# Kernel tuning notes

Measured on AMD Instinct MI355X. Metric: run time of the kernel, lower is better.

## Reference

```python
import jax, jax.numpy as jnp
import numpy as np

B, N, OBS_DIM = 64, 512, 128
HIDDEN_DIM, MESSAGE_DIM, ACTION_DIM = 256, 128, 16


def _dense_params(key, din, dout):
    kw, kb = jax.random.split(key)
    W = jax.random.normal(kw, (din, dout), jnp.float32) * 0.02
    b = jnp.zeros((dout,), jnp.float32)
    return W, b


def setup_inputs() -> dict:
    key = jax.random.key(0)
    ks = jax.random.split(key, 12)
    obs_batch = jax.random.normal(ks[0], (B, N, OBS_DIM), jnp.float32)
    dones_batch = jnp.zeros((B, N), jnp.bool_)
    We, be = _dense_params(ks[1], OBS_DIM, HIDDEN_DIM)
    Wc, bc = _dense_params(ks[2], HIDDEN_DIM, MESSAGE_DIM // 4)
    Wn, bn = _dense_params(ks[3], HIDDEN_DIM, MESSAGE_DIM // 2)
    Wb, bb = _dense_params(ks[4], HIDDEN_DIM, MESSAGE_DIM // 4)
    Wi, bi = _dense_params(ks[5], HIDDEN_DIM, 1)
    Wq, bq = _dense_params(ks[6], HIDDEN_DIM, MESSAGE_DIM)
    Wk, bk = _dense_params(ks[7], MESSAGE_DIM, MESSAGE_DIM)
    Wv, bv = _dense_params(ks[8], MESSAGE_DIM, MESSAGE_DIM)
    Wp, bp = _dense_params(ks[9], HIDDEN_DIM + MESSAGE_DIM, HIDDEN_DIM)
    Wa, ba = _dense_params(ks[10], HIDDEN_DIM, ACTION_DIM)
    Wcr, bcr = _dense_params(ks[11], HIDDEN_DIM, 1)
    return {"obs_batch": obs_batch, "dones_batch": dones_batch,
            "We": We, "be": be, "Wc": Wc, "bc": bc, "Wn": Wn, "bn": bn,
            "Wb": Wb, "bb": bb, "Wi": Wi, "bi": bi, "Wq": Wq, "bq": bq,
            "Wk": Wk, "bk": bk, "Wv": Wv, "bv": bv, "Wp": Wp, "bp": bp,
            "Wa": Wa, "ba": ba, "Wcr": Wcr, "bcr": bcr}


def reference(obs_batch, dones_batch, We, be, Wc, bc, Wn, bn, Wb, bb, Wi, bi,
              Wq, bq, Wk, bk, Wv, bv, Wp, bp, Wa, ba, Wcr, bcr):
    dense = lambda x, W, b: x @ W + b
    encoded = jax.nn.relu(dense(obs_batch, We, be))                 # [B,N,H]
    messages = jnp.concatenate([dense(encoded, Wc, bc),
                                dense(encoded, Wn, bn),
                                dense(encoded, Wb, bb)], axis=-1)   # [B,N,M]
    importance = jax.nn.sigmoid(dense(encoded, Wi, bi))             # [B,N,1]
    Q = dense(encoded, Wq, bq)
    K = dense(messages, Wk, bk)
    V = dense(messages, Wv, bv)
    scores = jnp.einsum('bqd,bkd->bqk', Q, K) / jnp.sqrt(jnp.float32(MESSAGE_DIM))
    importance_weights = importance * jnp.transpose(importance, (0, 2, 1))  # [B,N,N]
    scores = scores * importance_weights
    norms = jnp.linalg.norm(obs_batch, axis=-1, keepdims=True)      # [B,N,1]
    obs_sim = jnp.einsum('bid,bjd->bij', obs_batch, obs_batch)
    obs_sim = obs_sim / (norms + 1e-08)
    obs_sim = obs_sim / (jnp.transpose(norms, (0, 2, 1)) + 1e-08)
    scores = scores + obs_sim * 0.5
    attn = jax.nn.softmax(scores, axis=-1)
    aggregated = jnp.einsum('bqk,bkd->bqd', attn, V)                # [B,N,M]
    combined = jnp.concatenate([encoded, aggregated], axis=-1)
    x = jax.nn.relu(dense(combined, Wp, bp))
    logits = dense(x, Wa, ba)
    value = dense(x, Wcr, bcr).squeeze(-1)
    return (logits, value)
```

## Files before the change

### kernel.cpp

```cpp
#include <hip/hip_runtime.h>
#include <math.h>


typedef __attribute__((ext_vector_type(8))) short short8;
typedef __attribute__((ext_vector_type(4))) float f32x4;

#define RSQRT_D 0.08838834764831843f

__device__ __forceinline__ unsigned short f2bf(float f) {
  union { float f; unsigned u; } v; v.f = f;
  return (unsigned short)((v.u + 0x7FFFu + ((v.u >> 16) & 1u)) >> 16);
}
__device__ __forceinline__ float bf2f(unsigned short h) {
  union { unsigned u; float f; } v; v.u = ((unsigned)h) << 16;
  return v.f;
}
__device__ __forceinline__ unsigned pack2(float a, float b) {
  return (unsigned)f2bf(a) | ((unsigned)f2bf(b) << 16);
}

__device__ __forceinline__ int swz(int row, int chunk) {
  return row * 128 + ((chunk ^ ((row & 7) << 1)) << 3);
}

__global__ __launch_bounds__(256) void prep_w(
    const float* __restrict__ We, const float* __restrict__ Wq,
    const float* __restrict__ Wk, const float* __restrict__ Wv,
    const float* __restrict__ Wp, const float* __restrict__ Wc,
    const float* __restrict__ Wn, const float* __restrict__ Wb,
    const float* __restrict__ bc, const float* __restrict__ bn,
    const float* __restrict__ bb, const float* __restrict__ Wa,
    const float* __restrict__ Wcr, unsigned short* __restrict__ WeT,
    unsigned short* __restrict__ Wmq, unsigned short* __restrict__ Wkv,
    unsigned short* __restrict__ WpT, unsigned short* __restrict__ WaCrT,
    float* __restrict__ bm) {
  int idx = blockIdx.x * 256 + threadIdx.x;
  if (idx < 32768) {
    int n = idx >> 7, k = idx & 127;
    WeT[idx] = f2bf(We[k * 256 + n]);
  } else if (idx < 65536) {
    int i = idx - 32768;
    int d = i >> 8, h = i & 255;
    float v = (d < 32)   ? Wc[h * 32 + d]
            : (d < 96)   ? Wn[h * 64 + (d - 32)]
                         : Wb[h * 32 + (d - 96)];
    Wmq[i] = f2bf(v);
  } else if (idx < 98304) {
    int i = idx - 65536;
    int n = i >> 8, k = i & 255;
    Wmq[32768 + i] = f2bf(Wq[k * 128 + n]);
  } else if (idx < 114688) {
    int i = idx - 98304;
    int n = i >> 7, k = i & 127;
    Wkv[i] = f2bf(Wk[k * 128 + n]);
  } else if (idx < 131072) {
    int i = idx - 114688;
    int n = i >> 7, k = i & 127;
    Wkv[16384 + i] = f2bf(Wv[k * 128 + n]);
  } else if (idx < 229376) {
    int i = idx - 131072;
    int n = i / 384, k = i - n * 384;
    WpT[i] = f2bf(Wp[k * 256 + n]);
  } else if (idx < 237568) {
    int i = idx - 229376;
    int n = i >> 8, k = i & 255;
    float v = (n < 16) ? Wa[k * 16 + n] : (n == 16) ? Wcr[k] : 0.f;
    WaCrT[i] = f2bf(v);
  } else if (idx < 237696) {
    int i = idx - 237568;
    bm[i] = (i < 32) ? bc[i] : (i < 96) ? bn[i - 32] : bb[i - 96];
  }
}

__global__ __launch_bounds__(256) void prep_obs(
    const float* __restrict__ obs, unsigned short* __restrict__ obs_bf,
    unsigned short* __restrict__ As, unsigned short* __restrict__ Bs) {
  int t = blockIdx.x * 4 + (threadIdx.x >> 6);
  int lane = threadIdx.x & 63;
  const float* row = obs + (size_t)t * 128;
  float2 o = *(const float2*)(row + lane * 2);
  float s2 = o.x * o.x + o.y * o.y;
#pragma unroll
  for (int off = 1; off < 64; off <<= 1) s2 += __shfl_xor(s2, off);
  float inv = 1.f / (sqrtf(s2) + 1e-8f);
  ((unsigned*)obs_bf)[(size_t)t * 64 + lane] = pack2(o.x, o.y);
  ((unsigned*)As)[(size_t)t * 128 + 64 + lane] =
      pack2(o.x * 0.5f * inv, o.y * 0.5f * inv);
  ((unsigned*)Bs)[(size_t)t * 128 + 64 + lane] = pack2(o.x * inv, o.y * inv);
}

__global__ __launch_bounds__(256) void imp_kernel(
    const unsigned short* __restrict__ enc, const float* __restrict__ Wi,
    const float* __restrict__ bi, float* __restrict__ impA,
    float* __restrict__ impB) {
  int t = blockIdx.x * 4 + (threadIdx.x >> 6);
  int lane = threadIdx.x & 63;
  const unsigned* eu = (const unsigned*)(enc + (size_t)t * 256);
  unsigned u0 = eu[lane * 2], u1 = eu[lane * 2 + 1];
  float4 w = *(const float4*)(Wi + lane * 4);
  float s = bf2f((unsigned short)(u0 & 0xFFFF)) * w.x +
            bf2f((unsigned short)(u0 >> 16)) * w.y +
            bf2f((unsigned short)(u1 & 0xFFFF)) * w.z +
            bf2f((unsigned short)(u1 >> 16)) * w.w;
#pragma unroll
  for (int off = 1; off < 64; off <<= 1) s += __shfl_xor(s, off);
  if (lane == 0) {
    float sg = 1.0f / (1.0f + __expf(-(s + bi[0])));
    impA[t] = sg * RSQRT_D;
    impB[t] = sg;
  }
}

template <int MODE>
__device__ __forceinline__ void epi_store(unsigned short* out, int ldc,
                                          const float* bias,
                                          const float* scale, int rowb,
                                          int col, const f32x4& a) {
  const float bv = bias ? bias[col] : 0.f;
  if constexpr (MODE == 3) {
    unsigned short t0 = f2bf(a[0] + bv), t1 = f2bf(a[1] + bv);
    unsigned short t2 = f2bf(a[2] + bv), t3 = f2bf(a[3] + bv);
    uint2 o;
    o.x = (unsigned)t0 | ((unsigned)t1 << 16);
    o.y = (unsigned)t2 | ((unsigned)t3 << 16);
    *(uint2*)(out + ((size_t)(rowb >> 9) * 128 + col) * 512 + (rowb & 511)) = o;
  } else {
#pragma unroll
    for (int r = 0; r < 4; ++r) {
      float v = a[r] + bv;
      if constexpr (MODE == 1) v = fmaxf(v, 0.f);
      if constexpr (MODE == 2) v *= scale[rowb + r];
      out[(size_t)(rowb + r) * ldc + col] = f2bf(v);
    }
  }
}

template <int M0, int M1>
__global__ __launch_bounds__(256, 2) void gemm_dual(
    const unsigned short* __restrict__ A1, int lda1, int K1,
    const unsigned short* __restrict__ A2, int lda2, int Ktot,
    const unsigned short* __restrict__ Bt, int ldb,
    const float* __restrict__ bias0, const float* __restrict__ bias1,
    const float* __restrict__ scale, unsigned short* __restrict__ out0,
    int ldc0, unsigned short* __restrict__ out1, int ldc1, int xsplit) {
  __shared__ unsigned short Asr[64][72];
  __shared__ unsigned short Bsr[128][72];
  const int tid = threadIdx.x;
  const int lane = tid & 63, wave = tid >> 6;
  const int quad = lane >> 4, l16 = lane & 15;
  const int wm = wave & 1, wn = wave >> 1;
  const int bm = blockIdx.y * 64, bn = blockIdx.x * 128;

  f32x4 acc[2][4];
#pragma unroll
  for (int i = 0; i < 2; ++i)
#pragma unroll
    for (int j = 0; j < 4; ++j) acc[i][j] = (f32x4){0.f, 0.f, 0.f, 0.f};

  const int ar = tid >> 3, ac = tid & 7;
  for (int kt = 0; kt < Ktot; kt += 64) {
    const unsigned short* Asrc;
    int lda, kloc;
    if (kt < K1) { Asrc = A1; lda = lda1; kloc = kt; }
    else         { Asrc = A2; lda = lda2; kloc = kt - K1; }
#pragma unroll
    for (int it = 0; it < 2; ++it) {
      int r = ar + it * 32;
      uint4 v = *(const uint4*)(Asrc + (size_t)(bm + r) * lda + kloc + ac * 8);
      *(uint4*)&Asr[r][ac * 8] = v;
    }
#pragma unroll
    for (int it = 0; it < 4; ++it) {
      int r = ar + it * 32;
      uint4 v = *(const uint4*)(Bt + (size_t)(bn + r) * ldb + kt + ac * 8);
      *(uint4*)&Bsr[r][ac * 8] = v;
    }
    __syncthreads();
#pragma unroll
    for (int ks = 0; ks < 64; ks += 32) {
      short8 af[2], bfr[4];
#pragma unroll
      for (int i = 0; i < 2; ++i)
        af[i] = *(const short8*)&Asr[wm * 32 + i * 16 + l16][ks + quad * 8];
#pragma unroll
      for (int j = 0; j < 4; ++j)
        bfr[j] = *(const short8*)&Bsr[wn * 64 + j * 16 + l16][ks + quad * 8];
#pragma unroll
      for (int i = 0; i < 2; ++i)
#pragma unroll
        for (int j = 0; j < 4; ++j)
          acc[i][j] = __builtin_amdgcn_mfma_f32_16x16x32_bf16(af[i], bfr[j],
                                                              acc[i][j], 0, 0, 0);
    }
    __syncthreads();
  }
  const int colb = bn + wn * 64 + l16;
#pragma unroll
  for (int i = 0; i < 2; ++i) {
    const int rowb = bm + wm * 32 + i * 16 + quad * 4;
#pragma unroll
    for (int j = 0; j < 4; ++j) {
      const int col = colb + j * 16;
      if (col < xsplit)
        epi_store<M0>(out0, ldc0, bias0, scale, rowb, col, acc[i][j]);
      else
        epi_store<M1>(out1, ldc1, bias1, scale, rowb, col - xsplit, acc[i][j]);
    }
  }
}

__global__ __launch_bounds__(256, 3) void flash2(
    const unsigned short* __restrict__ As, const unsigned short* __restrict__ Bs,
    const unsigned short* __restrict__ vT, unsigned short* __restrict__ agg) {
  __shared__ unsigned short Ub[128 * 128];
  __shared__ unsigned short Pp[32 * 128];
  __shared__ float redm[2][32];
  __shared__ float reds[2][32];
  const int tid = threadIdx.x;
  const int lane = tid & 63, wave = tid >> 6;
  const int quad = lane >> 4, l16 = lane & 15;
  const int wm = wave & 1, wn = wave >> 1;
  const int b = blockIdx.x & 63;
  const int qt = blockIdx.x >> 6;
  const size_t tokA = (size_t)b * 512 + qt * 32;

  short8 af[8];
#pragma unroll
  for (int kc = 0; kc < 8; ++kc)
    af[kc] = *(const short8*)(As + (tokA + wm * 16 + l16) * 256 + kc * 32 +
                              quad * 8);

  f32x4 s[4][4];
#pragma unroll
  for (int kt = 0; kt < 4; ++kt)
#pragma unroll
    for (int nt = 0; nt < 4; ++nt) s[kt][nt] = (f32x4){0.f, 0.f, 0.f, 0.f};

  const int lr = tid >> 4, lc = tid & 15;

#pragma unroll
  for (int kt = 0; kt < 4; ++kt) {
#pragma unroll
    for (int kh = 0; kh < 2; ++kh) {
      __syncthreads();
#pragma unroll
      for (int it = 0; it < 8; ++it) {
        int r = lr + it * 16;
        *(uint4*)&Ub[swz(r, lc)] =
            *(const uint4*)(Bs + ((size_t)b * 512 + kt * 128 + r) * 256 +
                            kh * 128 + lc * 8);
      }
      __syncthreads();
#pragma unroll
      for (int kk = 0; kk < 4; ++kk) {
        short8 bfr[4];
#pragma unroll
        for (int nt = 0; nt < 4; ++nt) {
          int rrow = wn * 64 + nt * 16 + l16;
          bfr[nt] = *(const short8*)&Ub[swz(rrow, kk * 4 + quad)];
        }
#pragma unroll
        for (int nt = 0; nt < 4; ++nt)
          s[kt][nt] = __builtin_amdgcn_mfma_f32_16x16x32_bf16(
              af[kh * 4 + kk], bfr[nt], s[kt][nt], 0, 0, 0);
      }
    }
  }

  const int rbase = wm * 16 + quad * 4;
  float mt4[4];
#pragma unroll
  for (int r = 0; r < 4; ++r) {
    float mv = -1e30f;
#pragma unroll
    for (int kt = 0; kt < 4; ++kt)
#pragma unroll
      for (int nt = 0; nt < 4; ++nt) mv = fmaxf(mv, s[kt][nt][r]);
#pragma unroll
    for (int off = 1; off < 16; off <<= 1) mv = fmaxf(mv, __shfl_xor(mv, off));
    mt4[r] = mv;
  }
  if (l16 == 0) {
#pragma unroll
    for (int r = 0; r < 4; ++r) redm[wn][rbase + r] = mt4[r];
  }
  __syncthreads();
  float lsum[4];
#pragma unroll
  for (int r = 0; r < 4; ++r) {
    float mfull = fmaxf(mt4[r], redm[1 ^ wn][rbase + r]);
    float sum = 0.f;
#pragma unroll
    for (int kt = 0; kt < 4; ++kt)
#pragma unroll
      for (int nt = 0; nt < 4; ++nt) {
        float p = __expf(s[kt][nt][r] - mfull);
        s[kt][nt][r] = p;
        sum += p;
      }
#pragma unroll
    for (int off = 1; off < 16; off <<= 1) sum += __shfl_xor(sum, off);
    lsum[r] = sum;
  }
  if (l16 == 0) {
#pragma unroll
    for (int r = 0; r < 4; ++r) reds[wn][rbase + r] = lsum[r];
  }
  __syncthreads();
  float linv[4];
#pragma unroll
  for (int r = 0; r < 4; ++r)
    linv[r] = 1.0f / (lsum[r] + reds[1 ^ wn][rbase + r]);

  f32x4 oacc[4];
#pragma unroll
  for (int nt = 0; nt < 4; ++nt) oacc[nt] = (f32x4){0.f, 0.f, 0.f, 0.f};
#pragma unroll
  for (int vt = 0; vt < 4; ++vt) {
    __syncthreads();
#pragma unroll
    for (int nt = 0; nt < 4; ++nt)
#pragma unroll
      for (int r = 0; r < 4; ++r) {
        int row = rbase + r;
        int col = wn * 64 + nt * 16 + l16;
        Pp[row * 128 + (((col >> 3) ^ ((row & 7) << 1)) << 3) + (col & 7)] =
            f2bf(s[vt][nt][r]);
      }
#pragma unroll
    for (int it = 0; it < 8; ++it) {
      int r = lr + it * 16;
      *(uint4*)&Ub[swz(r, lc)] =
          *(const uint4*)(vT + ((size_t)b * 128 + r) * 512 + vt * 128 + lc * 8);
    }
    __syncthreads();
#pragma unroll
    for (int kk = 0; kk < 4; ++kk) {
      short8 pa = *(const short8*)&Pp[swz(wm * 16 + l16, kk * 4 + quad)];
#pragma unroll
      for (int nt = 0; nt < 4; ++nt) {
        int rrow = wn * 64 + nt * 16 + l16;
        short8 vb = *(const short8*)&Ub[swz(rrow, kk * 4 + quad)];
        oacc[nt] = __builtin_amdgcn_mfma_f32_16x16x32_bf16(pa, vb, oacc[nt],
                                                           0, 0, 0);
      }
    }
  }

#pragma unroll
  for (int nt = 0; nt < 4; ++nt) {
    const int col = wn * 64 + nt * 16 + l16;
#pragma unroll
    for (int r = 0; r < 4; ++r)
      agg[(tokA + rbase + r) * 128 + col] = f2bf(oacc[nt][r] * linv[r]);
  }
}

__global__ __launch_bounds__(256, 3) void xh_gemm(
    const unsigned short* __restrict__ A1, const unsigned short* __restrict__ A2,
    const unsigned short* __restrict__ WpT, const float* __restrict__ bp,
    const unsigned short* __restrict__ WaCrT, const float* __restrict__ ba,
    const float* __restrict__ bcr, float* __restrict__ logits,
    float* __restrict__ value) {
  __shared__ unsigned short Asr[32][72];
  __shared__ unsigned short Bsr[256][72];
  const int tid = threadIdx.x;
  const int lane = tid & 63, wave = tid >> 6;
  const int quad = lane >> 4, l16 = lane & 15;
  const int bm = blockIdx.x * 32;

  f32x4 acc[2][4];
#pragma unroll
  for (int i = 0; i < 2; ++i)
#pragma unroll
    for (int j = 0; j < 4; ++j) acc[i][j] = (f32x4){0.f, 0.f, 0.f, 0.f};

  const int ar = tid >> 3, ac = tid & 7;
  for (int kt = 0; kt < 384; kt += 64) {
    const unsigned short* Asrc;
    int lda, kloc;
    if (kt < 256) { Asrc = A1; lda = 256; kloc = kt; }
    else          { Asrc = A2; lda = 128; kloc = kt - 256; }
    *(uint4*)&Asr[ar][ac * 8] =
        *(const uint4*)(Asrc + (size_t)(bm + ar) * lda + kloc + ac * 8);
#pragma unroll
    for (int it = 0; it < 8; ++it) {
      int idx = tid + it * 256;
      int r = idx >> 3, c = idx & 7;
      *(uint4*)&Bsr[r][c * 8] = *(const uint4*)(WpT + (size_t)r * 384 + kt + c * 8);
    }
    __syncthreads();
#pragma unroll
    for (int kk = 0; kk < 2; ++kk) {
      short8 afr[2], bfr[4];
#pragma unroll
      for (int i = 0; i < 2; ++i)
        afr[i] = *(const short8*)&Asr[i * 16 + l16][kk * 32 + quad * 8];
#pragma unroll
      for (int j = 0; j < 4; ++j)
        bfr[j] = *(const short8*)&Bsr[wave * 64 + j * 16 + l16][kk * 32 + quad * 8];
#pragma unroll
      for (int i = 0; i < 2; ++i)
#pragma unroll
        for (int j = 0; j < 4; ++j)
          acc[i][j] = __builtin_amdgcn_mfma_f32_16x16x32_bf16(afr[i], bfr[j],
                                                              acc[i][j], 0, 0, 0);
    }
    __syncthreads();
  }
  unsigned short* xs = &Bsr[0][0];
#pragma unroll
  for (int i = 0; i < 2; ++i) {
    const int row = i * 16 + quad * 4;
#pragma unroll
    for (int j = 0; j < 4; ++j) {
      const int col = wave * 64 + j * 16 + l16;
      const float bv = bp[col];
#pragma unroll
      for (int r = 0; r < 4; ++r)
        xs[(row + r) * 264 + col] = f2bf(fmaxf(acc[i][j][r] + bv, 0.f));
    }
  }
  __syncthreads();
  const int wm2 = wave & 1, wn2 = wave >> 1;
  f32x4 hacc = (f32x4){0.f, 0.f, 0.f, 0.f};
#pragma unroll
  for (int kk = 0; kk < 8; ++kk) {
    short8 pa = *(const short8*)&xs[(wm2 * 16 + l16) * 264 + kk * 32 + quad * 8];
    short8 wb = *(const short8*)(WaCrT + (size_t)(wn2 * 16 + l16) * 256 +
                                 kk * 32 + quad * 8);
    hacc = __builtin_amdgcn_mfma_f32_16x16x32_bf16(pa, wb, hacc, 0, 0, 0);
  }
  const int n = wn2 * 16 + l16;
#pragma unroll
  for (int r = 0; r < 4; ++r) {
    const size_t tok = bm + wm2 * 16 + quad * 4 + r;
    if (n < 16)
      logits[tok * 16 + n] = hacc[r] + ba[n];
    else if (n == 16)
      value[tok] = hacc[r] + bcr[0];
  }
}

extern "C" void kernel_launch(void* const* d_in, const int* in_sizes, int n_in,
                              void* d_out, int out_size, void* d_ws,
                              size_t ws_size, hipStream_t stream) {
  const float* obs = (const float*)d_in[0];
  const float* We = (const float*)d_in[2];
  const float* be = (const float*)d_in[3];
  const float* Wc = (const float*)d_in[4];
  const float* bc = (const float*)d_in[5];
  const float* Wn = (const float*)d_in[6];
  const float* bn = (const float*)d_in[7];
  const float* Wb = (const float*)d_in[8];
  const float* bb = (const float*)d_in[9];
  const float* Wi = (const float*)d_in[10];
  const float* bi = (const float*)d_in[11];
  const float* Wq = (const float*)d_in[12];
  const float* bq = (const float*)d_in[13];
  const float* Wk = (const float*)d_in[14];
  const float* bk = (const float*)d_in[15];
  const float* Wv = (const float*)d_in[16];
  const float* bv = (const float*)d_in[17];
  const float* Wp = (const float*)d_in[18];
  const float* bp = (const float*)d_in[19];
  const float* Wa = (const float*)d_in[20];
  const float* ba = (const float*)d_in[21];
  const float* Wcr = (const float*)d_in[22];
  const float* bcr = (const float*)d_in[23];

  char* base = (char*)d_ws;
  unsigned short* enc_bf = (unsigned short*)(base);
  unsigned short* As     = (unsigned short*)(base + 16777216);
  unsigned short* Bs     = (unsigned short*)(base + 33554432);
  unsigned short* obsagg = (unsigned short*)(base + 50331648);
  unsigned short* msg_bf = (unsigned short*)(base + 58720256);
  unsigned short* vT     = (unsigned short*)(base + 75497472);
  float* impA            = (float*)(base + 83886080);
  float* impB            = (float*)(base + 84017152);
  unsigned short* WeT    = (unsigned short*)(base + 84148224);
  unsigned short* Wmq    = (unsigned short*)(base + 84213760);
  unsigned short* Wkv    = (unsigned short*)(base + 84344832);
  unsigned short* WpT    = (unsigned short*)(base + 84410368);
  float* bmb             = (float*)(base + 84606976);
  unsigned short* WaCrT  = (unsigned short*)(base + 84607488);

  prep_w<<<929, 256, 0, stream>>>(We, Wq, Wk, Wv, Wp, Wc, Wn, Wb, bc, bn, bb,
                                  Wa, Wcr, WeT, Wmq, Wkv, WpT, WaCrT, bmb);
  prep_obs<<<8192, 256, 0, stream>>>(obs, obsagg, As, Bs);

  gemm_dual<1, 1><<<dim3(2, 512), 256, 0, stream>>>(
      obsagg, 128, 128, nullptr, 0, 128, WeT, 128, be, be, nullptr, enc_bf,
      256, enc_bf, 256, 256);
  imp_kernel<<<8192, 256, 0, stream>>>(enc_bf, Wi, bi, impA, impB);

  gemm_dual<0, 2><<<dim3(2, 512), 256, 0, stream>>>(
      enc_bf, 256, 256, nullptr, 0, 256, Wmq, 256, bmb, bq, impA, msg_bf, 128,
      As, 256, 128);
  gemm_dual<2, 3><<<dim3(2, 512), 256, 0, stream>>>(
      msg_bf, 128, 128, nullptr, 0, 128, Wkv, 128, bk, bv, impB, Bs, 256, vT,
      0, 128);

  flash2<<<1024, 256, 0, stream>>>(As, Bs, vT, obsagg);

  xh_gemm<<<1024, 256, 0, stream>>>(enc_bf, obsagg, WpT, bp, WaCrT, ba, bcr,
                                    (float*)d_out, (float*)d_out + 524288);
}
```

Baseline: 223.2 us.

## Fuse prep kernels, fold importance into encoder GEMM, use direct-to-LDS loads

Merges the weight prep, obs prep, and output/importance initialisation into one launch. The encoder GEMM epilogue now computes the importance dot product and accumulates it with atomics, which removes the separate importance kernel; downstream GEMMs apply the sigmoid themselves. All GEMMs move to 128x128 tiles with global_load_lds into XOR-swizzled LDS, and the final projection splits N across blocks, atomically accumulating partial head outputs onto bias-initialised logits and value. The atomics make summation order nondeterministic, and the larger tiles halve the grid size.

```diff
diff --git a/kernel.cpp b/kernel.cpp
--- a/kernel.cpp
+++ b/kernel.cpp
@@ -6,237 +6,246 @@
 typedef __attribute__((ext_vector_type(4))) float f32x4;
 
 #define RSQRT_D 0.08838834764831843f
+#define MFMA __builtin_amdgcn_mfma_f32_16x16x32_bf16
 
 __device__ __forceinline__ unsigned short f2bf(float f) {
   union { float f; unsigned u; } v; v.f = f;
   return (unsigned short)((v.u + 0x7FFFu + ((v.u >> 16) & 1u)) >> 16);
 }
-__device__ __forceinline__ float bf2f(unsigned short h) {
-  union { unsigned u; float f; } v; v.u = ((unsigned)h) << 16;
-  return v.f;
-}
 __device__ __forceinline__ unsigned pack2(float a, float b) {
   return (unsigned)f2bf(a) | ((unsigned)f2bf(b) << 16);
 }
-
-__device__ __forceinline__ int swz(int row, int chunk) {
-  return row * 128 + ((chunk ^ ((row & 7) << 1)) << 3);
-}
-
-__global__ __launch_bounds__(256) void prep_w(
-    const float* __restrict__ We, const float* __restrict__ Wq,
-    const float* __restrict__ Wk, const float* __restrict__ Wv,
-    const float* __restrict__ Wp, const float* __restrict__ Wc,
-    const float* __restrict__ Wn, const float* __restrict__ Wb,
-    const float* __restrict__ bc, const float* __restrict__ bn,
-    const float* __restrict__ bb, const float* __restrict__ Wa,
-    const float* __restrict__ Wcr, unsigned short* __restrict__ WeT,
-    unsigned short* __restrict__ Wmq, unsigned short* __restrict__ Wkv,
-    unsigned short* __restrict__ WpT, unsigned short* __restrict__ WaCrT,
-    float* __restrict__ bm) {
-  int idx = blockIdx.x * 256 + threadIdx.x;
-  if (idx < 32768) {
-    int n = idx >> 7, k = idx & 127;
-    WeT[idx] = f2bf(We[k * 256 + n]);
-  } else if (idx < 65536) {
-    int i = idx - 32768;
-    int d = i >> 8, h = i & 255;
-    float v = (d < 32)   ? Wc[h * 32 + d]
-            : (d < 96)   ? Wn[h * 64 + (d - 32)]
-                         : Wb[h * 32 + (d - 96)];
-    Wmq[i] = f2bf(v);
-  } else if (idx < 98304) {
-    int i = idx - 65536;
-    int n = i >> 8, k = i & 255;
-    Wmq[32768 + i] = f2bf(Wq[k * 128 + n]);
-  } else if (idx < 114688) {
-    int i = idx - 98304;
-    int n = i >> 7, k = i & 127;
-    Wkv[i] = f2bf(Wk[k * 128 + n]);
-  } else if (idx < 131072) {
-    int i = idx - 114688;
-    int n = i >> 7, k = i & 127;
-    Wkv[16384 + i] = f2bf(Wv[k * 128 + n]);
-  } else if (idx < 229376) {
-    int i = idx - 131072;
-    int n = i / 384, k = i - n * 384;
-    WpT[i] = f2bf(Wp[k * 256 + n]);
-  } else if (idx < 237568) {
-    int i = idx - 229376;
-    int n = i >> 8, k = i & 255;
-    float v = (n < 16) ? Wa[k * 16 + n] : (n == 16) ? Wcr[k] : 0.f;
-    WaCrT[i] = f2bf(v);
-  } else if (idx < 237696) {
-    int i = idx - 237568;
-    bm[i] = (i < 32) ? bc[i] : (i < 96) ? bn[i - 32] : bb[i - 96];
-  }
-}
-
-__global__ __launch_bounds__(256) void prep_obs(
-    const float* __restrict__ obs, unsigned short* __restrict__ obs_bf,
-    unsigned short* __restrict__ As, unsigned short* __restrict__ Bs) {
-  int t = blockIdx.x * 4 + (threadIdx.x >> 6);
-  int lane = threadIdx.x & 63;
-  const float* row = obs + (size_t)t * 128;
-  float2 o = *(const float2*)(row + lane * 2);
-  float s2 = o.x * o.x + o.y * o.y;
-#pragma unroll
-  for (int off = 1; off < 64; off <<= 1) s2 += __shfl_xor(s2, off);
-  float inv = 1.f / (sqrtf(s2) + 1e-8f);
-  ((unsigned*)obs_bf)[(size_t)t * 64 + lane] = pack2(o.x, o.y);
-  ((unsigned*)As)[(size_t)t * 128 + 64 + lane] =
-      pack2(o.x * 0.5f * inv, o.y * 0.5f * inv);
-  ((unsigned*)Bs)[(size_t)t * 128 + 64 + lane] = pack2(o.x * inv, o.y * inv);
-}
-
-__global__ __launch_bounds__(256) void imp_kernel(
-    const unsigned short* __restrict__ enc, const float* __restrict__ Wi,
-    const float* __restrict__ bi, float* __restrict__ impA,
-    float* __restrict__ impB) {
-  int t = blockIdx.x * 4 + (threadIdx.x >> 6);
-  int lane = threadIdx.x & 63;
-  const unsigned* eu = (const unsigned*)(enc + (size_t)t * 256);
-  unsigned u0 = eu[lane * 2], u1 = eu[lane * 2 + 1];
-  float4 w = *(const float4*)(Wi + lane * 4);
-  float s = bf2f((unsigned short)(u0 & 0xFFFF)) * w.x +
-            bf2f((unsigned short)(u0 >> 16)) * w.y +
-            bf2f((unsigned short)(u1 & 0xFFFF)) * w.z +
-            bf2f((unsigned short)(u1 >> 16)) * w.w;
-#pragma unroll
-  for (int off = 1; off < 64; off <<= 1) s += __shfl_xor(s, off);
-  if (lane == 0) {
-    float sg = 1.0f / (1.0f + __expf(-(s + bi[0])));
-    impA[t] = sg * RSQRT_D;
-    impB[t] = sg;
-  }
-}
-
-template <int MODE>
-__device__ __forceinline__ void epi_store(unsigned short* out, int ldc,
-                                          const float* bias,
-                                          const float* scale, int rowb,
-                                          int col, const f32x4& a) {
-  const float bv = bias ? bias[col] : 0.f;
+__device__ __forceinline__ short8 ld8(const unsigned short* p) {
+  return *(const short8*)p;
+}
+__device__ __forceinline__ void gl16(const unsigned short* g,
+                                     unsigned short* l) {
+  __builtin_amdgcn_global_load_lds(
+      (const __attribute__((address_space(1))) unsigned int*)(const void*)g,
+      (__attribute__((address_space(3))) unsigned int*)(void*)l, 16, 0, 0);
+}
+
+__global__ __launch_bounds__(256) void prep_all(
+    const float* __restrict__ obs, const float* __restrict__ We,
+    const float* __restrict__ Wq, const float* __restrict__ Wk,
+    const float* __restrict__ Wv, const float* __restrict__ Wp,
+    const float* __restrict__ Wc, const float* __restrict__ Wn,
+    const float* __restrict__ Wb, const float* __restrict__ bc,
+    const float* __restrict__ bn, const float* __restrict__ bb,
+    const float* __restrict__ Wa, const float* __restrict__ Wcr,
+    const float* __restrict__ ba, const float* __restrict__ bcr,
+    unsigned short* __restrict__ WeT, unsigned short* __restrict__ Wmq,
+    unsigned short* __restrict__ Wkv, unsigned short* __restrict__ WpT,
+    unsigned short* __restrict__ WaCrT, float* __restrict__ bm,
+    unsigned short* __restrict__ obs_bf, unsigned short* __restrict__ As,
+    unsigned short* __restrict__ Bs, float* __restrict__ logits,
+    float* __restrict__ value, float* __restrict__ imp_raw) {
+  const int bid = blockIdx.x, tid = threadIdx.x;
+  if (bid < 929) {
+    int idx = bid * 256 + tid;
+    if (idx < 32768) {
+      int n = idx >> 7, k = idx & 127;
+      WeT[idx] = f2bf(We[k * 256 + n]);
+    } else if (idx < 65536) {
+      int i = idx - 32768;
+      int d = i >> 8, h = i & 255;
+      float v = (d < 32)   ? Wc[h * 32 + d]
+              : (d < 96)   ? Wn[h * 64 + (d - 32)]
+                           : Wb[h * 32 + (d - 96)];
+      Wmq[i] = f2bf(v);
+    } else if (idx < 98304) {
+      int i = idx - 65536;
+      int n = i >> 8, k = i & 255;
+      Wmq[32768 + i] = f2bf(Wq[k * 128 + n]);
+    } else if (idx < 114688) {
+      int i = idx - 98304;
+      int n = i >> 7, k = i & 127;
+      Wkv[i] = f2bf(Wk[k * 128 + n]);
+    } else if (idx < 131072) {
+      int i = idx - 114688;
+      int n = i >> 7, k = i & 127;
+      Wkv[16384 + i] = f2bf(Wv[k * 128 + n]);
+    } else if (idx < 229376) {
+      int i = idx - 131072;
+      int n = i / 384, k = i - n * 384;
+      WpT[i] = f2bf(Wp[k * 256 + n]);
+    } else if (idx < 237568) {
+      int i = idx - 229376;
+      int n = i >> 8, k = i & 255;
+      float v = (n < 16) ? Wa[k * 16 + n] : (n == 16) ? Wcr[k] : 0.f;
+      WaCrT[i] = f2bf(v);
+    } else if (idx < 237696) {
+      int i = idx - 237568;
+      bm[i] = (i < 32) ? bc[i] : (i < 96) ? bn[i - 32] : bb[i - 96];
+    }
+  } else if (bid < 9121) {
+    int t = (bid - 929) * 4 + (tid >> 6);
+    int lane = tid & 63;
+    const float* row = obs + (size_t)t * 128;
+    float2 o = *(const float2*)(row + lane * 2);
+    float s2 = o.x * o.x + o.y * o.y;
+#pragma unroll
+    for (int off = 1; off < 64; off <<= 1) s2 += __shfl_xor(s2, off);
+    float inv = 1.f / (sqrtf(s2) + 1e-8f);
+    ((unsigned*)obs_bf)[(size_t)t * 64 + lane] = pack2(o.x, o.y);
+    ((unsigned*)As)[(size_t)t * 128 + 64 + lane] =
+        pack2(o.x * 0.5f * inv, o.y * 0.5f * inv);
+    ((unsigned*)Bs)[(size_t)t * 128 + 64 + lane] = pack2(o.x * inv, o.y * inv);
+  } else if (bid < 11297) {
+    int i = (bid - 9121) * 256 + tid;
+    if (i < 524288) logits[i] = ba[i & 15];
+    else value[i - 524288] = bcr[0];
+  } else {
+    imp_raw[(bid - 11297) * 256 + tid] = 0.f;
+  }
+}
+
+template <int MODE, int IMP>
+__device__ __forceinline__ void emit(unsigned short* out, int ldc,
+                                     const float* bias, const float* sg,
+                                     int rowb, int col, const f32x4& a,
+                                     float* ip, const float* Wi, int gcol) {
+  const float bv = bias[col];
   if constexpr (MODE == 3) {
-    unsigned short t0 = f2bf(a[0] + bv), t1 = f2bf(a[1] + bv);
-    unsigned short t2 = f2bf(a[2] + bv), t3 = f2bf(a[3] + bv);
     uint2 o;
-    o.x = (unsigned)t0 | ((unsigned)t1 << 16);
-    o.y = (unsigned)t2 | ((unsigned)t3 << 16);
+    o.x = pack2(a[0] + bv, a[1] + bv);
+    o.y = pack2(a[2] + bv, a[3] + bv);
     *(uint2*)(out + ((size_t)(rowb >> 9) * 128 + col) * 512 + (rowb & 511)) = o;
   } else {
+    float wv = 0.f;
+    if constexpr (IMP) wv = Wi[gcol];
 #pragma unroll
     for (int r = 0; r < 4; ++r) {
       float v = a[r] + bv;
       if constexpr (MODE == 1) v = fmaxf(v, 0.f);
-      if constexpr (MODE == 2) v *= scale[rowb + r];
+      if constexpr (MODE == 2) v *= sg[r];
       out[(size_t)(rowb + r) * ldc + col] = f2bf(v);
-    }
-  }
-}
-
-template <int M0, int M1>
-__global__ __launch_bounds__(256, 2) void gemm_dual(
+      if constexpr (IMP) ip[r] += v * wv;
+    }
+  }
+}
+
+template <int M0, int M1, int IMP>
+__global__ __launch_bounds__(256, 2) void gemm_t(
     const unsigned short* __restrict__ A1, int lda1, int K1,
     const unsigned short* __restrict__ A2, int lda2, int Ktot,
     const unsigned short* __restrict__ Bt, int ldb,
     const float* __restrict__ bias0, const float* __restrict__ bias1,
-    const float* __restrict__ scale, unsigned short* __restrict__ out0,
-    int ldc0, unsigned short* __restrict__ out1, int ldc1, int xsplit) {
-  __shared__ unsigned short Asr[64][72];
-  __shared__ unsigned short Bsr[128][72];
-  const int tid = threadIdx.x;
-  const int lane = tid & 63, wave = tid >> 6;
+    const float* __restrict__ raw, const float* __restrict__ bi, float mult,
+    const float* __restrict__ Wi, float* __restrict__ imp_out,
+    unsigned short* __restrict__ out0, int ldc0,
+    unsigned short* __restrict__ out1, int ldc1, int xsplit) {
+  __shared__ unsigned short Asr[8192];
+  __shared__ unsigned short Bsr[8192];
+  const int tid = threadIdx.x, lane = tid & 63, wave = tid >> 6;
   const int quad = lane >> 4, l16 = lane & 15;
   const int wm = wave & 1, wn = wave >> 1;
-  const int bm = blockIdx.y * 64, bn = blockIdx.x * 128;
-
-  f32x4 acc[2][4];
-#pragma unroll
-  for (int i = 0; i < 2; ++i)
+  const int bm = blockIdx.y * 128, bn = blockIdx.x * 128;
+  const int srow = tid >> 3, slc = tid & 7;
+
+  f32x4 acc[4][4];
+#pragma unroll
+  for (int i = 0; i < 4; ++i)
 #pragma unroll
     for (int j = 0; j < 4; ++j) acc[i][j] = (f32x4){0.f, 0.f, 0.f, 0.f};
 
-  const int ar = tid >> 3, ac = tid & 7;
   for (int kt = 0; kt < Ktot; kt += 64) {
-    const unsigned short* Asrc;
+    const unsigned short* Ap;
     int lda, kloc;
-    if (kt < K1) { Asrc = A1; lda = lda1; kloc = kt; }
-    else         { Asrc = A2; lda = lda2; kloc = kt - K1; }
-#pragma unroll
-    for (int it = 0; it < 2; ++it) {
-      int r = ar + it * 32;
-      uint4 v = *(const uint4*)(Asrc + (size_t)(bm + r) * lda + kloc + ac * 8);
-      *(uint4*)&Asr[r][ac * 8] = v;
-    }
-#pragma unroll
-    for (int it = 0; it < 4; ++it) {
-      int r = ar + it * 32;
-      uint4 v = *(const uint4*)(Bt + (size_t)(bn + r) * ldb + kt + ac * 8);
-      *(uint4*)&Bsr[r][ac * 8] = v;
+    if (kt < K1) { Ap = A1; lda = lda1; kloc = kt; }
+    else         { Ap = A2; lda = lda2; kloc = kt - K1; }
+#pragma unroll
+    for (int i = 0; i < 4; ++i) {
+      int row = i * 32 + srow;
+      gl16(Ap + (size_t)(bm + row) * lda + kloc + ((slc ^ (row & 7)) << 3),
+           Asr + i * 2048 + wave * 512);
+      gl16(Bt + (size_t)(bn + row) * ldb + kt + ((slc ^ (row & 7)) << 3),
+           Bsr + i * 2048 + wave * 512);
     }
     __syncthreads();
 #pragma unroll
-    for (int ks = 0; ks < 64; ks += 32) {
-      short8 af[2], bfr[4];
-#pragma unroll
-      for (int i = 0; i < 2; ++i)
-        af[i] = *(const short8*)&Asr[wm * 32 + i * 16 + l16][ks + quad * 8];
-#pragma unroll
-      for (int j = 0; j < 4; ++j)
-        bfr[j] = *(const short8*)&Bsr[wn * 64 + j * 16 + l16][ks + quad * 8];
-#pragma unroll
-      for (int i = 0; i < 2; ++i)
-#pragma unroll
-        for (int j = 0; j < 4; ++j)
-          acc[i][j] = __builtin_amdgcn_mfma_f32_16x16x32_bf16(af[i], bfr[j],
-                                                              acc[i][j], 0, 0, 0);
+    for (int ks = 0; ks < 2; ++ks) {
+      short8 af[4], bf[4];
+#pragma unroll
+      for (int mi = 0; mi < 4; ++mi) {
+        int row = wm * 64 + mi * 16 + l16;
+        af[mi] = *(const short8*)&Asr[row * 64 + (((ks * 4 + quad) ^ (row & 7)) << 3)];
+      }
+#pragma unroll
+      for (int ni = 0; ni < 4; ++ni) {
+        int row = wn * 64 + ni * 16 + l16;
+        bf[ni] = *(const short8*)&Bsr[row * 64 + (((ks * 4 + quad) ^ (row & 7)) << 3)];
+      }
+#pragma unroll
+      for (int mi = 0; mi < 4; ++mi)
+#pragma unroll
+        for (int ni = 0; ni < 4; ++ni)
+          acc[mi][ni] = MFMA(af[mi], bf[ni], acc[mi][ni], 0, 0, 0);
     }
     __syncthreads();
   }
-  const int colb = bn + wn * 64 + l16;
-#pragma unroll
-  for (int i = 0; i < 2; ++i) {
-    const int rowb = bm + wm * 32 + i * 16 + quad * 4;
-#pragma unroll
-    for (int j = 0; j < 4; ++j) {
-      const int col = colb + j * 16;
+
+  float bi0 = 0.f;
+  if constexpr (M0 == 2 || M1 == 2) bi0 = bi[0];
+#pragma unroll
+  for (int mi = 0; mi < 4; ++mi) {
+    const int rowb = bm + wm * 64 + mi * 16 + quad * 4;
+    float sg[4] = {0.f, 0.f, 0.f, 0.f};
+    if constexpr (M0 == 2 || M1 == 2) {
+#pragma unroll
+      for (int r = 0; r < 4; ++r)
+        sg[r] = mult / (1.f + __expf(-(raw[rowb + r] + bi0)));
+    }
+    float ip[4] = {0.f, 0.f, 0.f, 0.f};
+#pragma unroll
+    for (int ni = 0; ni < 4; ++ni) {
+      const int col = bn + wn * 64 + ni * 16 + l16;
       if (col < xsplit)
-        epi_store<M0>(out0, ldc0, bias0, scale, rowb, col, acc[i][j]);
+        emit<M0, IMP>(out0, ldc0, bias0, sg, rowb, col, acc[mi][ni], ip, Wi, col);
       else
-        epi_store<M1>(out1, ldc1, bias1, scale, rowb, col - xsplit, acc[i][j]);
-    }
-  }
-}
-
-__global__ __launch_bounds__(256, 3) void flash2(
+        emit<M1, 0>(out1, ldc1, bias1, sg, rowb, col - xsplit, acc[mi][ni],
+                    nullptr, nullptr, 0);
+    }
+    if constexpr (IMP) {
+#pragma unroll
+      for (int r = 0; r < 4; ++r) {
+#pragma unroll
+        for (int off = 1; off < 16; off <<= 1)
+          ip[r] += __shfl_xor(ip[r], off);
+      }
+      if (l16 == 0) {
+#pragma unroll
+        for (int r = 0; r < 4; ++r) atomicAdd(&imp_out[rowb + r], ip[r]);
+      }
+    }
+  }
+}
+
+__global__ __launch_bounds__(256, 3) void flash4(
     const unsigned short* __restrict__ As, const unsigned short* __restrict__ Bs,
     const unsigned short* __restrict__ vT, unsigned short* __restrict__ agg) {
-  __shared__ unsigned short Ub[128 * 128];
-  __shared__ unsigned short Pp[32 * 128];
+  __shared__ unsigned short Ub[16384];
+  __shared__ unsigned short Pp[4096];
   __shared__ float redm[2][32];
   __shared__ float reds[2][32];
-  const int tid = threadIdx.x;
-  const int lane = tid & 63, wave = tid >> 6;
+  const int tid = threadIdx.x, lane = tid & 63, wave = tid >> 6;
   const int quad = lane >> 4, l16 = lane & 15;
   const int wm = wave & 1, wn = wave >> 1;
   const int b = blockIdx.x & 63;
   const int qt = blockIdx.x >> 6;
-  const size_t tokA = (size_t)b * 512 + qt * 32;
+  const size_t tok0 = (size_t)b * 512 + qt * 32;
+  const int srow = tid >> 4, slc = tid & 15;
 
   short8 af[8];
 #pragma unroll
   for (int kc = 0; kc < 8; ++kc)
-    af[kc] = *(const short8*)(As + (tokA + wm * 16 + l16) * 256 + kc * 32 +
-                              quad * 8);
+    af[kc] = ld8(As + (tok0 + wm * 16 + l16) * 256 + kc * 32 + quad * 8);
 
   f32x4 s[4][4];
 #pragma unroll
   for (int kt = 0; kt < 4; ++kt)
 #pragma unroll
     for (int nt = 0; nt < 4; ++nt) s[kt][nt] = (f32x4){0.f, 0.f, 0.f, 0.f};
-
-  const int lr = tid >> 4, lc = tid & 15;
 
 #pragma unroll
   for (int kt = 0; kt < 4; ++kt) {
@@ -244,11 +253,11 @@
     for (int kh = 0; kh < 2; ++kh) {
       __syncthreads();
 #pragma unroll
-      for (int it = 0; it < 8; ++it) {
-        int r = lr + it * 16;
-        *(uint4*)&Ub[swz(r, lc)] =
-            *(const uint4*)(Bs + ((size_t)b * 512 + kt * 128 + r) * 256 +
-                            kh * 128 + lc * 8);
+      for (int i = 0; i < 8; ++i) {
+        int row = i * 16 + srow;
+        gl16(Bs + ((size_t)b * 512 + kt * 128 + row) * 256 + kh * 128 +
+                 ((slc ^ (row & 15)) << 3),
+             Ub + i * 2048 + wave * 512);
       }
       __syncthreads();
 #pragma unroll
@@ -256,19 +265,18 @@
         short8 bfr[4];
 #pragma unroll
         for (int nt = 0; nt < 4; ++nt) {
-          int rrow = wn * 64 + nt * 16 + l16;
-          bfr[nt] = *(const short8*)&Ub[swz(rrow, kk * 4 + quad)];
+          int rr = wn * 64 + nt * 16 + l16;
+          bfr[nt] = *(const short8*)&Ub[rr * 128 + (((kk * 4 + quad) ^ (rr & 15)) << 3)];
         }
 #pragma unroll
         for (int nt = 0; nt < 4; ++nt)
-          s[kt][nt] = __builtin_amdgcn_mfma_f32_16x16x32_bf16(
-              af[kh * 4 + kk], bfr[nt], s[kt][nt], 0, 0, 0);
+          s[kt][nt] = MFMA(af[kh * 4 + kk], bfr[nt], s[kt][nt], 0, 0, 0);
       }
     }
   }
 
   const int rbase = wm * 16 + quad * 4;
-  float mt4[4];
+  float mt[4];
 #pragma unroll
   for (int r = 0; r < 4; ++r) {
     float mv = -1e30f;
@@ -278,17 +286,17 @@
       for (int nt = 0; nt < 4; ++nt) mv = fmaxf(mv, s[kt][nt][r]);
 #pragma unroll
     for (int off = 1; off < 16; off <<= 1) mv = fmaxf(mv, __shfl_xor(mv, off));
-    mt4[r] = mv;
+    mt[r] = mv;
   }
   if (l16 == 0) {
 #pragma unroll
-    for (int r = 0; r < 4; ++r) redm[wn][rbase + r] = mt4[r];
+    for (int r = 0; r < 4; ++r) redm[wn][rbase + r] = mt[r];
   }
   __syncthreads();
   float lsum[4];
 #pragma unroll
   for (int r = 0; r < 4; ++r) {
-    float mfull = fmaxf(mt4[r], redm[1 ^ wn][rbase + r]);
+    float mfull = fmaxf(mt[r], redm[1 ^ wn][rbase + r]);
     float sum = 0.f;
 #pragma unroll
     for (int kt = 0; kt < 4; ++kt)
@@ -319,126 +327,153 @@
   for (int vt = 0; vt < 4; ++vt) {
     __syncthreads();
 #pragma unroll
-    for (int nt = 0; nt < 4; ++nt)
+    for (int nt = 0; nt < 4; ++nt) {
+      const int col = wn * 64 + nt * 16 + l16;
 #pragma unroll
       for (int r = 0; r < 4; ++r) {
-        int row = rbase + r;
-        int col = wn * 64 + nt * 16 + l16;
-        Pp[row * 128 + (((col >> 3) ^ ((row & 7) << 1)) << 3) + (col & 7)] =
+        const int row = rbase + r;
+        Pp[row * 128 + (((col >> 3) ^ (row & 15)) << 3) + (col & 7)] =
             f2bf(s[vt][nt][r]);
       }
-#pragma unroll
-    for (int it = 0; it < 8; ++it) {
-      int r = lr + it * 16;
-      *(uint4*)&Ub[swz(r, lc)] =
-          *(const uint4*)(vT + ((size_t)b * 128 + r) * 512 + vt * 128 + lc * 8);
+    }
+#pragma unroll
+    for (int i = 0; i < 8; ++i) {
+      int row = i * 16 + srow;
+      gl16(vT + ((size_t)b * 128 + row) * 512 + vt * 128 +
+               ((slc ^ (row & 15)) << 3),
+           Ub + i * 2048 + wave * 512);
     }
     __syncthreads();
 #pragma unroll
     for (int kk = 0; kk < 4; ++kk) {
-      short8 pa = *(const short8*)&Pp[swz(wm * 16 + l16, kk * 4 + quad)];
+      const int prow = wm * 16 + l16;
+      short8 pa = *(const short8*)&Pp[prow * 128 + (((kk * 4 + quad) ^ (prow & 15)) << 3)];
 #pragma unroll
       for (int nt = 0; nt < 4; ++nt) {
-        int rrow = wn * 64 + nt * 16 + l16;
-        short8 vb = *(const short8*)&Ub[swz(rrow, kk * 4 + quad)];
-        oacc[nt] = __builtin_amdgcn_mfma_f32_16x16x32_bf16(pa, vb, oacc[nt],
-                                                           0, 0, 0);
-      }
-    }
-  }
-
+        int rr = wn * 64 + nt * 16 + l16;
+        short8 vb = *(const short8*)&Ub[rr * 128 + (((kk * 4 + quad) ^ (rr & 15)) << 3)];
+        oacc[nt] = MFMA(pa, vb, oacc[nt], 0, 0, 0);
+      }
+    }
+  }
 #pragma unroll
   for (int nt = 0; nt < 4; ++nt) {
     const int col = wn * 64 + nt * 16 + l16;
 #pragma unroll
     for (int r = 0; r < 4; ++r)
-      agg[(tokA + rbase + r) * 128 + col] = f2bf(oacc[nt][r] * linv[r]);
-  }
-}
-
-__global__ __launch_bounds__(256, 3) void xh_gemm(
-    const unsigned short* __restrict__ A1, const unsigned short* __restrict__ A2,
+      agg[(tok0 + rbase + r) * 128 + col] = f2bf(oacc[nt][r] * linv[r]);
+  }
+}
+
+__global__ __launch_bounds__(256, 2) void xh_gemm(
+    const unsigned short* __restrict__ enc, const unsigned short* __restrict__ agg,
     const unsigned short* __restrict__ WpT, const float* __restrict__ bp,
-    const unsigned short* __restrict__ WaCrT, const float* __restrict__ ba,
-    const float* __restrict__ bcr, float* __restrict__ logits,
+    const unsigned short* __restrict__ WaCrT, float* __restrict__ logits,
     float* __restrict__ value) {
-  __shared__ unsigned short Asr[32][72];
-  __shared__ unsigned short Bsr[256][72];
-  const int tid = threadIdx.x;
-  const int lane = tid & 63, wave = tid >> 6;
+  __shared__ unsigned short sm[16384];
+  unsigned short* Asr = sm;
+  unsigned short* Bsr = sm + 8192;
+  const int tid = threadIdx.x, lane = tid & 63, wave = tid >> 6;
   const int quad = lane >> 4, l16 = lane & 15;
-  const int bm = blockIdx.x * 32;
-
-  f32x4 acc[2][4];
+  const int wm = wave & 1, wn = wave >> 1;
+  const int bm = blockIdx.y * 128, bn = blockIdx.x * 128;
+  const int srow = tid >> 3, slc = tid & 7;
+
+  f32x4 acc[4][4];
+#pragma unroll
+  for (int i = 0; i < 4; ++i)
+#pragma unroll
+    for (int j = 0; j < 4; ++j) acc[i][j] = (f32x4){0.f, 0.f, 0.f, 0.f};
+
+  for (int kt = 0; kt < 384; kt += 64) {
+    const unsigned short* Ap;
+    int lda, kloc;
+    if (kt < 256) { Ap = enc; lda = 256; kloc = kt; }
+    else          { Ap = agg; lda = 128; kloc = kt - 256; }
+#pragma unroll
+    for (int i = 0; i < 4; ++i) {
+      int row = i * 32 + srow;
+      gl16(Ap + (size_t)(bm + row) * lda + kloc + ((slc ^ (row & 7)) << 3),
+           Asr + i * 2048 + wave * 512);
+      gl16(WpT + (size_t)(bn + row) * 384 + kt + ((slc ^ (row & 7)) << 3),
+           Bsr + i * 2048 + wave * 512);
+    }
+    __syncthreads();
+#pragma unroll
+    for (int ks = 0; ks < 2; ++ks) {
+      short8 af[4], bf[4];
+#pragma unroll
+      for (int mi = 0; mi < 4; ++mi) {
+        int row = wm * 64 + mi * 16 + l16;
+        af[mi] = *(const short8*)&Asr[row * 64 + (((ks * 4 + quad) ^ (row & 7)) << 3)];
+      }
+#pragma unroll
+      for (int ni = 0; ni < 4; ++ni) {
+        int row = wn * 64 + ni * 16 + l16;
+        bf[ni] = *(const short8*)&Bsr[row * 64 + (((ks * 4 + quad) ^ (row & 7)) << 3)];
+      }
+#pragma unroll
+      for (int mi = 0; mi < 4; ++mi)
+#pragma unroll
+        for (int ni = 0; ni < 4; ++ni)
+          acc[mi][ni] = MFMA(af[mi], bf[ni], acc[mi][ni], 0, 0, 0);
+    }
+    __syncthreads();
+  }
+
+#pragma unroll
+  for (int mi = 0; mi < 4; ++mi) {
+    const int row = wm * 64 + mi * 16 + quad * 4;
+#pragma unroll
+    for (int ni = 0; ni < 4; ++ni) {
+      const int colc = wn * 64 + ni * 16 + l16;
+      const float bv = bp[bn + colc];
+#pragma unroll
+      for (int r = 0; r < 4; ++r) {
+        float v = fmaxf(acc[mi][ni][r] + bv, 0.f);
+        sm[(row + r) * 128 + (((colc >> 3) ^ ((row + r) & 15)) << 3) + (colc & 7)] =
+            f2bf(v);
+      }
+    }
+  }
+  __syncthreads();
+
+  f32x4 h[2][2];
 #pragma unroll
   for (int i = 0; i < 2; ++i)
 #pragma unroll
-    for (int j = 0; j < 4; ++j) acc[i][j] = (f32x4){0.f, 0.f, 0.f, 0.f};
-
-  const int ar = tid >> 3, ac = tid & 7;
-  for (int kt = 0; kt < 384; kt += 64) {
-    const unsigned short* Asrc;
-    int lda, kloc;
-    if (kt < 256) { Asrc = A1; lda = 256; kloc = kt; }
-    else          { Asrc = A2; lda = 128; kloc = kt - 256; }
-    *(uint4*)&Asr[ar][ac * 8] =
-        *(const uint4*)(Asrc + (size_t)(bm + ar) * lda + kloc + ac * 8);
-#pragma unroll
-    for (int it = 0; it < 8; ++it) {
-      int idx = tid + it * 256;
-      int r = idx >> 3, c = idx & 7;
-      *(uint4*)&Bsr[r][c * 8] = *(const uint4*)(WpT + (size_t)r * 384 + kt + c * 8);
-    }
-    __syncthreads();
-#pragma unroll
-    for (int kk = 0; kk < 2; ++kk) {
-      short8 afr[2], bfr[4];
-#pragma unroll
-      for (int i = 0; i < 2; ++i)
-        afr[i] = *(const short8*)&Asr[i * 16 + l16][kk * 32 + quad * 8];
-#pragma unroll
-      for (int j = 0; j < 4; ++j)
-        bfr[j] = *(const short8*)&Bsr[wave * 64 + j * 16 + l16][kk * 32 + quad * 8];
-#pragma unroll
-      for (int i = 0; i < 2; ++i)
-#pragma unroll
-        for (int j = 0; j < 4; ++j)
-          acc[i][j] = __builtin_amdgcn_mfma_f32_16x16x32_bf16(afr[i], bfr[j],
-                                                              acc[i][j], 0, 0, 0);
-    }
-    __syncthreads();
-  }
-  unsigned short* xs = &Bsr[0][0];
-#pragma unroll
-  for (int i = 0; i < 2; ++i) {
-    const int row = i * 16 + quad * 4;
-#pragma unroll
-    for (int j = 0; j < 4; ++j) {
-      const int col = wave * 64 + j * 16 + l16;
-      const float bv = bp[col];
-#pragma unroll
-      for (int r = 0; r < 4; ++r)
-        xs[(row + r) * 264 + col] = f2bf(fmaxf(acc[i][j][r] + bv, 0.f));
-    }
-  }
-  __syncthreads();
-  const int wm2 = wave & 1, wn2 = wave >> 1;
-  f32x4 hacc = (f32x4){0.f, 0.f, 0.f, 0.f};
-#pragma unroll
-  for (int kk = 0; kk < 8; ++kk) {
-    short8 pa = *(const short8*)&xs[(wm2 * 16 + l16) * 264 + kk * 32 + quad * 8];
-    short8 wb = *(const short8*)(WaCrT + (size_t)(wn2 * 16 + l16) * 256 +
-                                 kk * 32 + quad * 8);
-    hacc = __builtin_amdgcn_mfma_f32_16x16x32_bf16(pa, wb, hacc, 0, 0, 0);
-  }
-  const int n = wn2 * 16 + l16;
-#pragma unroll
-  for (int r = 0; r < 4; ++r) {
-    const size_t tok = bm + wm2 * 16 + quad * 4 + r;
-    if (n < 16)
-      logits[tok * 16 + n] = hacc[r] + ba[n];
-    else if (n == 16)
-      value[tok] = hacc[r] + bcr[0];
+    for (int j = 0; j < 2; ++j) h[i][j] = (f32x4){0.f, 0.f, 0.f, 0.f};
+#pragma unroll
+  for (int kc = 0; kc < 4; ++kc) {
+    short8 xa[2], wb[2];
+#pragma unroll
+    for (int hm = 0; hm < 2; ++hm) {
+      int row = wave * 32 + hm * 16 + l16;
+      xa[hm] = *(const short8*)&sm[row * 128 + (((kc * 4 + quad) ^ (row & 15)) << 3)];
+    }
+#pragma unroll
+    for (int hn = 0; hn < 2; ++hn)
+      wb[hn] = ld8(WaCrT + (size_t)(hn * 16 + l16) * 256 + bn + kc * 32 + quad * 8);
+#pragma unroll
+    for (int hm = 0; hm < 2; ++hm)
+#pragma unroll
+      for (int hn = 0; hn < 2; ++hn)
+        h[hm][hn] = MFMA(xa[hm], wb[hn], h[hm][hn], 0, 0, 0);
+  }
+#pragma unroll
+  for (int hm = 0; hm < 2; ++hm) {
+#pragma unroll
+    for (int hn = 0; hn < 2; ++hn) {
+      const int n = hn * 16 + l16;
+#pragma unroll
+      for (int r = 0; r < 4; ++r) {
+        const int grow = bm + wave * 32 + hm * 16 + quad * 4 + r;
+        if (n < 16)
+          atomicAdd(&logits[(size_t)grow * 16 + n], h[hm][hn][r]);
+        else if (n == 16)
+          atomicAdd(&value[grow], h[hm][hn][r]);
+      }
+    }
   }
 }
 
@@ -476,8 +511,7 @@
   unsigned short* obsagg = (unsigned short*)(base + 50331648);
   unsigned short* msg_bf = (unsigned short*)(base + 58720256);
   unsigned short* vT     = (unsigned short*)(base + 75497472);
-  float* impA            = (float*)(base + 83886080);
-  float* impB            = (float*)(base + 84017152);
+  float* imp_raw         = (float*)(base + 83886080);
   unsigned short* WeT    = (unsigned short*)(base + 84148224);
   unsigned short* Wmq    = (unsigned short*)(base + 84213760);
   unsigned short* Wkv    = (unsigned short*)(base + 84344832);
@@ -485,24 +519,26 @@
   float* bmb             = (float*)(base + 84606976);
   unsigned short* WaCrT  = (unsigned short*)(base + 84607488);
 
-  prep_w<<<929, 256, 0, stream>>>(We, Wq, Wk, Wv, Wp, Wc, Wn, Wb, bc, bn, bb,
-                                  Wa, Wcr, WeT, Wmq, Wkv, WpT, WaCrT, bmb);
-  prep_obs<<<8192, 256, 0, stream>>>(obs, obsagg, As, Bs);
-
-  gemm_dual<1, 1><<<dim3(2, 512), 256, 0, stream>>>(
-      obsagg, 128, 128, nullptr, 0, 128, WeT, 128, be, be, nullptr, enc_bf,
-      256, enc_bf, 256, 256);
-  imp_kernel<<<8192, 256, 0, stream>>>(enc_bf, Wi, bi, impA, impB);
-
-  gemm_dual<0, 2><<<dim3(2, 512), 256, 0, stream>>>(
-      enc_bf, 256, 256, nullptr, 0, 256, Wmq, 256, bmb, bq, impA, msg_bf, 128,
-      As, 256, 128);
-  gemm_dual<2, 3><<<dim3(2, 512), 256, 0, stream>>>(
-      msg_bf, 128, 128, nullptr, 0, 128, Wkv, 128, bk, bv, impB, Bs, 256, vT,
-      0, 128);
-
-  flash2<<<1024, 256, 0, stream>>>(As, Bs, vT, obsagg);
-
-  xh_gemm<<<1024, 256, 0, stream>>>(enc_bf, obsagg, WpT, bp, WaCrT, ba, bcr,
-                                    (float*)d_out, (float*)d_out + 524288);
-}
+  float* logits = (float*)d_out;
+  float* value = (float*)d_out + 524288;
+
+  prep_all<<<11425, 256, 0, stream>>>(obs, We, Wq, Wk, Wv, Wp, Wc, Wn, Wb, bc,
+                                      bn, bb, Wa, Wcr, ba, bcr, WeT, Wmq, Wkv,
+                                      WpT, WaCrT, bmb, obsagg, As, Bs, logits,
+                                      value, imp_raw);
+
+  gemm_t<1, 1, 1><<<dim3(2, 256), 256, 0, stream>>>(
+      obsagg, 128, 128, nullptr, 0, 128, WeT, 128, be, be, nullptr, nullptr,
+      0.f, Wi, imp_raw, enc_bf, 256, enc_bf, 256, 256);
+  gemm_t<0, 2, 0><<<dim3(2, 256), 256, 0, stream>>>(
+      enc_bf, 256, 256, nullptr, 0, 256, Wmq, 256, bmb, bq, imp_raw, bi,
+      RSQRT_D, nullptr, nullptr, msg_bf, 128, As, 256, 128);
+  gemm_t<2, 3, 0><<<dim3(2, 256), 256, 0, stream>>>(
+      msg_bf, 128, 128, nullptr, 0, 128, Wkv, 128, bk, bv, imp_raw, bi, 1.0f,
+      nullptr, nullptr, Bs, 256, vT, 0, 128);
+
+  flash4<<<1024, 256, 0, stream>>>(As, Bs, vT, obsagg);
+
+  xh_gemm<<<dim3(2, 256), 256, 0, stream>>>(enc_bf, obsagg, WpT, bp, WaCrT,
+                                            logits, value);
+}
```

New measurement: 199.7 us. 1.12x faster.
